# Kernel optimization log

Measured on AMD Instinct MI355X. Metric: run time of the kernel, lower is better.

The kernel has to match this reference:

```python
import jax, jax.numpy as jnp
import numpy as np

N, T, D, H, DA = 128, 256, 512, 512, 4


def setup_inputs() -> dict:
    key = jax.random.key(0)
    k1, k2, k3, k4, k5, k6 = jax.random.split(key, 6)
    x = jax.random.normal(k1, (N, T, D), dtype=jnp.float32)
    A = jax.random.normal(k2, (N, H, DA, DA), dtype=jnp.float32)
    Wx = jax.random.normal(k3, (D, 4 * H), dtype=jnp.float32) / np.sqrt(D).astype(np.float32)
    Wh = jax.random.normal(k4, (H, 4 * H), dtype=jnp.float32) / np.sqrt(H).astype(np.float32)
    Wattn = jax.random.normal(k5, (H, 4 * H), dtype=jnp.float32) / np.sqrt(H).astype(np.float32)
    b = jnp.zeros((4 * H,), dtype=jnp.float32)
    return {"x": x, "A": A, "Wx": Wx, "Wh": Wh, "Wattn": Wattn, "b": b}


def _attn(prev_h, A_flat, scale):
    # prev_h: (N,H), A_flat: (N,H,P) with P = DA*DA
    scores = jnp.einsum('nh,nhp->np', prev_h, A_flat) * scale      # (N,P)
    w = jax.nn.softmax(scores, axis=-1)                             # (N,P)
    attn = jnp.einsum('nhp,np->nh', A_flat, w)                      # (N,H)
    return attn


def reference(x, A, Wx, Wh, Wattn, b):
    n, t, d = x.shape
    h_dim = A.shape[1]
    scale = 1.0 / jnp.sqrt(jnp.asarray(h_dim, dtype=x.dtype))
    A_flat = A.reshape(n, h_dim, -1)
    h0 = jnp.mean(A, axis=(2, 3))  # (N,H)
    c0 = h0
    xs = jnp.moveaxis(x, 1, 0)     # (T,N,D)

    def step(carry, x_t):
        prev_h, prev_c = carry
        attn = _attn(prev_h, A_flat, scale)
        a = x_t @ Wx + prev_h @ Wh + attn @ Wattn + b  # (N,4H)
        i, f, o, g = jnp.split(a, 4, axis=-1)
        next_c = jax.nn.sigmoid(f) * prev_c + jax.nn.sigmoid(i) * jnp.tanh(g)
        next_h = jax.nn.sigmoid(o) * jnp.tanh(next_c)
        return (next_h, next_c), next_h

    _, hs = jax.lax.scan(step, (h0, c0), xs)  # hs: (T,N,H)
    return jnp.moveaxis(hs, 0, 1)             # (N,T,H)
```

## Files before the change

### kernel.cpp

```cpp
#include <hip/hip_runtime.h>
#include <hip/hip_bf16.h>

typedef __bf16 bf16_t;
typedef __bf16 bf16x8 __attribute__((ext_vector_type(8)));
typedef float  f32x4  __attribute__((ext_vector_type(4)));

#define N_    128
#define T_    256
#define D_    512
#define H_    512
#define G4    2048
#define ZB_ELEMS 131072
#define XF_PER_T 65536
#define WB_PER_CB 32768

__device__ __forceinline__ int zidx(int k, int n) {
  return ((((k >> 5) * 8 + (n >> 4)) * 64) + ((k >> 3) & 3) * 16 + (n & 15)) * 8 + (k & 7);
}

__device__ __forceinline__ float sigf(float x) { return 1.f / (1.f + __expf(-x)); }
__device__ __forceinline__ float tanhfast(float x) {
  float e = __expf(2.f * x);
  return 1.f - 2.f / (e + 1.f);
}

__device__ __forceinline__ bf16x8 ld_frag_llc(const bf16_t* p) {
  unsigned long long lo = __hip_atomic_load((const unsigned long long*)p,
      __ATOMIC_RELAXED, __HIP_MEMORY_SCOPE_AGENT);
  unsigned long long hi = __hip_atomic_load(((const unsigned long long*)p) + 1,
      __ATOMIC_RELAXED, __HIP_MEMORY_SCOPE_AGENT);
  union { unsigned long long q[2]; bf16x8 v; } u; u.q[0] = lo; u.q[1] = hi; return u.v;
}
__device__ __forceinline__ float ld_f32_llc(const float* p) {
  return __hip_atomic_load(p, __ATOMIC_RELAXED, __HIP_MEMORY_SCOPE_AGENT);
}
__device__ __forceinline__ void st_u32_llc(unsigned int* p, unsigned int v) {
  __hip_atomic_store(p, v, __ATOMIC_RELAXED, __HIP_MEMORY_SCOPE_AGENT);
}
__device__ __forceinline__ int ld_i32_llc(const int* p) {
  return __hip_atomic_load(p, __ATOMIC_RELAXED, __HIP_MEMORY_SCOPE_AGENT);
}
__device__ __forceinline__ unsigned int pack2bf(float lo, float hi) {
  union { bf16_t h[2]; unsigned int u; } q;
  q.h[0] = (bf16_t)lo; q.h[1] = (bf16_t)hi; return q.u;
}

__global__ void prepW_kernel(const float* __restrict__ Wh, const float* __restrict__ Wx,
                             bf16_t* __restrict__ Wb) {
  int cb = blockIdx.x >> 1, kq = blockIdx.x & 1;
  int tt = threadIdx.x;
  int hl = tt & 7, gate = (tt >> 3) & 3, ko = tt >> 5;
  int oc = gate * H_ + cb * 8 + hl;
  int jpl = hl * 4 + gate;
  int wcl = jpl >> 4, c = jpl & 15;
  for (int kb = kq * 64; kb < kq * 64 + 64; kb++) {
    int k = kb * 8 + ko;
    float v = (k < 512) ? Wh[(size_t)k * G4 + oc] : Wx[(size_t)(k - 512) * G4 + oc];
    int kk = k >> 5, ch = (k >> 3) & 3, e = k & 7;
    Wb[(size_t)cb * WB_PER_CB + (((kk * 2 + wcl) * 64) + ch * 16 + c) * 8 + e] = (bf16_t)v;
  }
}

__global__ void prepX_kernel(const float* __restrict__ x, bf16_t* __restrict__ Xf) {
  int gid = blockIdx.x * 256 + threadIdx.x;
  int e8 = gid & 63;
  int n  = (gid >> 6) & 127;
  int t  = gid >> 13;
  int k  = e8 * 8;
  const float* xp = x + ((size_t)n * T_ + t) * D_ + k;
  union { bf16_t b[8]; bf16x8 v; } u;
#pragma unroll
  for (int e = 0; e < 8; e++) u.b[e] = (bf16_t)xp[e];
  int idx = ((k >> 5) * 8 + (n >> 4)) * 64 + ((k >> 3) & 3) * 16 + (n & 15);
  ((bf16x8*)(Xf + (size_t)t * XF_PER_T))[idx] = u.v;
}

__global__ void prepA_kernel(const float* __restrict__ A, const float* __restrict__ x,
                             bf16_t* __restrict__ A_sc, float* __restrict__ cbuf,
                             bf16_t* __restrict__ Zb, float* __restrict__ S,
                             int* __restrict__ bar) {
  __shared__ float a_ld[8192];
  __shared__ float h0s[512];
  __shared__ float redb[256 * 16];
  int n = blockIdx.x, tid = threadIdx.x;
  if (n == 0 && tid < 144) bar[tid * 32] = 0;
  if (tid < 16) S[2048 + n * 16 + tid] = 0.f;
  for (int i = tid; i < 8192; i += 256) a_ld[i] = A[(size_t)n * 8192 + i];
  __syncthreads();
  for (int h = tid; h < H_; h += 256) {
    float s = 0.f;
#pragma unroll
    for (int p = 0; p < 16; p++) s += a_ld[h * 16 + p];
    s *= (1.f / 16.f);
    h0s[h] = s;
    cbuf[n * H_ + h] = s;
    Zb[zidx(h, n)] = (bf16_t)s;
  }
  for (int d = tid; d < D_; d += 256)
    Zb[zidx(512 + d, n)] = (bf16_t)x[(size_t)n * T_ * D_ + d];
  for (int idx = tid; idx < 8192; idx += 256) {
    int k = idx >> 4, p = idx & 15;
    A_sc[(size_t)n * 8192 + ((k >> 3) * 16 + p) * 8 + (k & 7)] = (bf16_t)a_ld[idx];
  }
  __syncthreads();
  float part[16];
#pragma unroll
  for (int p = 0; p < 16; p++) part[p] = 0.f;
  for (int h = tid; h < H_; h += 256) {
    float hv = h0s[h];
#pragma unroll
    for (int p = 0; p < 16; p++) part[p] += hv * a_ld[h * 16 + p];
  }
#pragma unroll
  for (int p = 0; p < 16; p++) redb[tid * 16 + p] = part[p];
  __syncthreads();
  if (tid < 16) {
    float s = 0.f;
    for (int i = 0; i < 256; i++) s += redb[i * 16 + tid];
    S[n * 16 + tid] = s;
  }
}

__global__ void __launch_bounds__(256) prepB_kernel(const float* __restrict__ Wattn,
                             const bf16_t* __restrict__ A_sc, bf16_t* __restrict__ Bg) {
  __shared__ bf16_t Al[8192];
  int n = blockIdx.x >> 2, jpQ = blockIdx.x & 3;
  int tid = threadIdx.x, p = tid & 15, jg = tid >> 4;
  for (int i = tid; i < 1024; i += 256)
    ((bf16x8*)Al)[i] = ((const bf16x8*)(A_sc + (size_t)n * 8192))[i];
  __syncthreads();
  int cbb = jpQ * 16 + jg;
  float acc[32];
#pragma unroll
  for (int j = 0; j < 32; j++) acc[j] = 0.f;
  for (int k = 0; k < 512; k++) {
    float a = (float)Al[((k >> 3) * 16 + p) * 8 + (k & 7)];
    const float* wr = Wattn + (size_t)k * G4 + cbb * 8;
#pragma unroll
    for (int gate = 0; gate < 4; gate++) {
      const float4* w4 = (const float4*)(wr + gate * H_);
      float4 wa = w4[0], wb = w4[1];
      acc[0 * 4 + gate] += a * wa.x; acc[1 * 4 + gate] += a * wa.y;
      acc[2 * 4 + gate] += a * wa.z; acc[3 * 4 + gate] += a * wa.w;
      acc[4 * 4 + gate] += a * wb.x; acc[5 * 4 + gate] += a * wb.y;
      acc[6 * 4 + gate] += a * wb.z; acc[7 * 4 + gate] += a * wb.w;
    }
  }
  bf16_t* dst = Bg + (((size_t)n * 64 + cbb) * 32) * 16 + p;
#pragma unroll
  for (int jj = 0; jj < 32; jj++) dst[jj * 16] = (bf16_t)acc[jj];
}

__device__ __forceinline__ void gridbar(int* gbase, int leaf, int g0l) {
  __syncthreads();
  if (threadIdx.x == 0) {
    int my = __hip_atomic_fetch_add(gbase + leaf * 32, 1, __ATOMIC_RELAXED, __HIP_MEMORY_SCOPE_AGENT);
    bool rootwin = false;
    if ((my & 7) == 7) {
      int r = __hip_atomic_fetch_add(gbase + 8 * 32, 1, __ATOMIC_RELAXED, __HIP_MEMORY_SCOPE_AGENT);
      if ((r & 7) == 7) {
        rootwin = true;
#pragma unroll
        for (int l = 0; l < 8; l++)
          st_u32_llc((unsigned int*)(gbase + (9 + l) * 32), (unsigned int)(g0l + 1));
      }
    }
    if (!rootwin) {
      while (ld_i32_llc(gbase + (9 + leaf) * 32) == g0l) __builtin_amdgcn_s_sleep(1);
    }
  }
  __syncthreads();
}

template<int USE_XF>
__global__ void __launch_bounds__(256, 2)
lstm_kernel(const bf16_t* __restrict__ Xf, const bf16_t* __restrict__ A_sc,
            const bf16_t* __restrict__ Wb, const bf16_t* __restrict__ Bg,
            const float* __restrict__ bvec, const float* __restrict__ cbuf,
            bf16_t* __restrict__ Zb, float* __restrict__ S,
            float* __restrict__ out, int* __restrict__ bar,
            const float* __restrict__ x) {
  __shared__ bf16_t Wl[32768];
  __shared__ f32x4 red[4][2][64];
  __shared__ float hsh[16 * 9];
  __shared__ float wls[16 * 17];

  const int wg = blockIdx.x, tid = threadIdx.x;
  const int cb = wg >> 3;
  const int grp = (wg & 7) ^ ((wg >> 3) & 7) ^ ((wg >> 6) & 7);
  const int wave = tid >> 6, lane = tid & 63;
  const int s  = grp * 16 + (lane & 15);
  const int hcE = cb * 8 + wave * 4 + (lane >> 4);
  const int jpE = cb * 32 + wave * 16 + (lane & 15);
  const float bias_l = (wave < 2) ? bvec[(jpE & 3) * H_ + (jpE >> 2)] : 0.f;
  const int jl = wave * 16 + (lane & 15);
  const int leaf = cb >> 3;
  int* gbase = bar + grp * 18 * 32;
  const int kkb = wave * 8;

  {
    const bf16x8* src = (const bf16x8*)(Wb + (size_t)cb * WB_PER_CB);
    bf16x8* dst = (bf16x8*)Wl;
    for (int i = tid; i < 4096; i += 256) dst[i] = src[i];
  }
  float creg = (wave < 2) ? cbuf[s * H_ + hcE] : 0.f;
  __syncthreads();

  int cur = 0;
  for (int t = 0; t < T_; t++) {
    const bf16_t* Zc = Zb + cur * ZB_ELEMS;
    bf16_t* Zn = Zb + (cur ^ 1) * ZB_ELEMS;
    const int cur3 = t % 3, nxt3 = (t + 1) % 3, z3 = (t + 2) % 3;

    int g0l = 0;
    if (tid == 0) g0l = ld_i32_llc(gbase + (9 + leaf) * 32);
    asm volatile("" ::: "memory");

    if (tid < 4) st_u32_llc((unsigned int*)(S + z3 * 2048 + grp * 256 + cb * 4 + tid), 0u);

    if (!USE_XF && t + 1 < T_ && tid < 64) {
      int nl = tid >> 2, e2 = (tid & 3) * 2;
      int n = grp * 16 + nl;
      const float* xp = x + ((size_t)n * T_ + (t + 1)) * D_ + cb * 8 + e2;
      st_u32_llc((unsigned int*)(Zn + zidx(512 + cb * 8 + e2, n)), pack2bf(xp[0], xp[1]));
    }

    bf16x8 afrag[8];
    if (USE_XF && wave >= 2) {
      const bf16x8* xf = (const bf16x8*)(Xf + (size_t)t * XF_PER_T);
#pragma unroll
      for (int i = 0; i < 8; i++)
        afrag[i] = xf[((kkb - 16 + i) * 8 + grp) * 64 + lane];
    } else {
#pragma unroll
      for (int i = 0; i < 8; i++)
        afrag[i] = ld_frag_llc(Zc + ((size_t)((kkb + i) * 8 + grp) * 64 + lane) * 8);
    }

    if ((tid & 63) < 4) {
      int nl = wave * 4 + (tid & 63);
      int ng = grp * 16 + nl;
      float r[16];
#pragma unroll
      for (int p = 0; p < 16; p++)
        r[p] = ld_f32_llc(S + cur3 * 2048 + ng * 16 + p) * 0.044194173824159216f;
      float m = r[0];
#pragma unroll
      for (int p = 1; p < 16; p++) m = fmaxf(m, r[p]);
      float ssum = 0.f;
#pragma unroll
      for (int p = 0; p < 16; p++) { r[p] = __expf(r[p] - m); ssum += r[p]; }
      float inv = 1.f / ssum;
#pragma unroll
      for (int p = 0; p < 16; p++) wls[nl * 17 + p] = r[p] * inv;
    }

    f32x4 acc0 = {0.f, 0.f, 0.f, 0.f}, acc1 = {0.f, 0.f, 0.f, 0.f};
    {
      const bf16x8* Wf = (const bf16x8*)Wl;
#pragma unroll
      for (int i = 0; i < 8; i++) {
        int kk = kkb + i;
        acc0 = __builtin_amdgcn_mfma_f32_16x16x32_bf16(afrag[i], Wf[(kk * 2 + 0) * 64 + lane], acc0, 0, 0, 0);
        acc1 = __builtin_amdgcn_mfma_f32_16x16x32_bf16(afrag[i], Wf[(kk * 2 + 1) * 64 + lane], acc1, 0, 0, 0);
      }
    }
    red[wave][0][lane] = acc0;
    red[wave][1][lane] = acc1;
    __syncthreads();

    if (wave < 2) {
      f32x4 fa = red[0][wave][lane];
#pragma unroll
      for (int w = 1; w < 4; w++) {
        f32x4 o = red[w][wave][lane];
        fa[0] += o[0]; fa[1] += o[1]; fa[2] += o[2]; fa[3] += o[3];
      }
      const int nl0 = (lane >> 4) << 2;
#pragma unroll
      for (int rp = 0; rp < 4; rp++) {
        int nl = nl0 + rp;
        const bf16x8* bl = (const bf16x8*)(Bg +
            (((size_t)(grp * 16 + nl) * 64 + cb) * 32 + jl) * 16);
        bf16x8 b0 = bl[0], b1 = bl[1];
        const float* wn = wls + nl * 17;
        float add = 0.f;
#pragma unroll
        for (int p = 0; p < 8; p++) add += wn[p] * (float)b0[p];
#pragma unroll
        for (int p = 0; p < 8; p++) add += wn[8 + p] * (float)b1[p];
        fa[rp] += add + bias_l;
      }

      float gv[4] = {0.f, 0.f, 0.f, 0.f};
      const int srcbase = ((lane >> 2) & 3) * 16 + (lane >> 4) * 4;
#pragma unroll
      for (int rp = 0; rp < 4; rp++) {
        float v = fa[rp];
#pragma unroll
        for (int g = 0; g < 4; g++) {
          float sv = __shfl(v, srcbase + g, 64);
          if ((lane & 3) == rp) gv[g] = sv;
        }
      }

      float si = sigf(gv[0]), sf = sigf(gv[1]), so = sigf(gv[2]);
      float cn = sf * creg + si * tanhfast(gv[3]);
      float hn = so * tanhfast(cn);
      creg = cn;
      __builtin_nontemporal_store(hn, out + ((size_t)s * T_ + t) * H_ + hcE);

      union { bf16_t h; unsigned short u; } cvt; cvt.h = (bf16_t)hn;
      unsigned int hbits = cvt.u;
      unsigned int other = __shfl(hbits, (lane + 16) & 63, 64);
      if (((lane >> 4) & 1) == 0)
        st_u32_llc((unsigned int*)(Zn + zidx(hcE, s)), hbits | (other << 16));
      hsh[(s & 15) * 9 + (hcE & 7)] = hn;
    }
    __syncthreads();

    if (t + 1 < T_) {
      int nl = tid >> 4, p = tid & 15;
      int ng = grp * 16 + nl;
      const bf16x8 av = *(const bf16x8*)(A_sc + ((size_t)ng * 64 + cb) * 128 + p * 8);
      float part = 0.f;
#pragma unroll
      for (int c = 0; c < 8; c++) part += hsh[nl * 9 + c] * (float)av[c];
      atomicAdd(S + nxt3 * 2048 + ng * 16 + p, part);
    }

    gridbar(gbase, leaf, g0l);
    cur ^= 1;
  }
}

extern "C" void kernel_launch(void* const* d_in, const int* in_sizes, int n_in,
                              void* d_out, int out_size, void* d_ws, size_t ws_size,
                              hipStream_t stream) {
  const float* x     = (const float*)d_in[0];
  const float* A     = (const float*)d_in[1];
  const float* Wx    = (const float*)d_in[2];
  const float* Wh    = (const float*)d_in[3];
  const float* Wattn = (const float*)d_in[4];
  const float* bv    = (const float*)d_in[5];
  float* out = (float*)d_out;

  char* ws = (char*)d_ws;
  const size_t BAR_OFF = 0;
  const size_t S_OFF   = 32768;
  const size_t CB_OFF  = 57344;
  const size_t ZB_OFF  = 319488;
  const size_t ASC_OFF = 843776;
  const size_t WB_OFF  = 2940928;
  const size_t BG_OFF  = 7135232;
  const size_t XF_OFF  = 15523840;
  const size_t WS_BASE = 15523840;
  const size_t WS_XF   = 49078272;
  if (ws_size < WS_BASE) return;
  const bool use_xf = (ws_size >= WS_XF);

  int*    bar  = (int*)(ws + BAR_OFF);
  float*  S    = (float*)(ws + S_OFF);
  float*  cbuf = (float*)(ws + CB_OFF);
  bf16_t* Zb   = (bf16_t*)(ws + ZB_OFF);
  bf16_t* A_sc = (bf16_t*)(ws + ASC_OFF);
  bf16_t* Wb   = (bf16_t*)(ws + WB_OFF);
  bf16_t* Bg   = (bf16_t*)(ws + BG_OFF);
  bf16_t* Xf   = (bf16_t*)(ws + XF_OFF);

  prepW_kernel<<<dim3(128), dim3(256), 0, stream>>>(Wh, Wx, Wb);
  prepA_kernel<<<dim3(128), dim3(256), 0, stream>>>(A, x, A_sc, cbuf, Zb, S, bar);
  prepB_kernel<<<dim3(512), dim3(256), 0, stream>>>(Wattn, A_sc, Bg);
  if (use_xf) {
    prepX_kernel<<<dim3(8192), dim3(256), 0, stream>>>(x, Xf);
    lstm_kernel<1><<<dim3(512), dim3(256), 0, stream>>>(Xf, A_sc, Wb, Bg, bv, cbuf, Zb, S, out, bar, x);
  } else {
    lstm_kernel<0><<<dim3(512), dim3(256), 0, stream>>>(Xf, A_sc, Wb, Bg, bv, cbuf, Zb, S, out, bar, x);
  }
}
```

Measured before the change: 1.902 ms.

## Use two-wave workgroups with full-K MFMA per wave and split score accumulators

Each workgroup drops from four waves splitting K with a shared-memory reduction to two waves that each own one 16-column output tile and run all 32 K-steps. This removes the LDS reduction of partial accumulators, and every wave now does gate math instead of only half of them. The attention score buffer is split into 8 partitions indexed by cb&7, which spreads atomicAdd contention; readers then sum the 8 partials before the softmax. In exchange, each wave carries a longer serial MFMA chain and more fragment registers, occupancy drops, and score reads grow eightfold, which could lengthen the per-step critical path.

```diff
diff --git a/kernel.cpp b/kernel.cpp
--- a/kernel.cpp
+++ b/kernel.cpp
@@ -13,6 +13,7 @@
 #define ZB_ELEMS 131072
 #define XF_PER_T 65536
 #define WB_PER_CB 32768
+#define SPH 16384
 
 __device__ __forceinline__ int zidx(int k, int n) {
   return ((((k >> 5) * 8 + (n >> 4)) * 64) + ((k >> 3) & 3) * 16 + (n & 15)) * 8 + (k & 7);
@@ -84,7 +85,11 @@
   __shared__ float redb[256 * 16];
   int n = blockIdx.x, tid = threadIdx.x;
   if (n == 0 && tid < 144) bar[tid * 32] = 0;
-  if (tid < 16) S[2048 + n * 16 + tid] = 0.f;
+  if (tid < 128) S[SPH + (tid >> 4) * 2048 + n * 16 + (tid & 15)] = 0.f;
+  if (tid >= 128 && tid < 240) {
+    int q = 1 + ((tid - 128) >> 4);
+    S[q * 2048 + n * 16 + (tid & 15)] = 0.f;
+  }
   for (int i = tid; i < 8192; i += 256) a_ld[i] = A[(size_t)n * 8192 + i];
   __syncthreads();
   for (int h = tid; h < H_; h += 256) {
@@ -173,7 +178,7 @@
 }
 
 template<int USE_XF>
-__global__ void __launch_bounds__(256, 2)
+__global__ void __launch_bounds__(128, 1)
 lstm_kernel(const bf16_t* __restrict__ Xf, const bf16_t* __restrict__ A_sc,
             const bf16_t* __restrict__ Wb, const bf16_t* __restrict__ Bg,
             const float* __restrict__ bvec, const float* __restrict__ cbuf,
@@ -181,7 +186,7 @@
             float* __restrict__ out, int* __restrict__ bar,
             const float* __restrict__ x) {
   __shared__ bf16_t Wl[32768];
-  __shared__ f32x4 red[4][2][64];
+  __shared__ float sraw[16 * 17];
   __shared__ float hsh[16 * 9];
   __shared__ float wls[16 * 17];
 
@@ -192,18 +197,17 @@
   const int s  = grp * 16 + (lane & 15);
   const int hcE = cb * 8 + wave * 4 + (lane >> 4);
   const int jpE = cb * 32 + wave * 16 + (lane & 15);
-  const float bias_l = (wave < 2) ? bvec[(jpE & 3) * H_ + (jpE >> 2)] : 0.f;
+  const float bias_l = bvec[(jpE & 3) * H_ + (jpE >> 2)];
   const int jl = wave * 16 + (lane & 15);
   const int leaf = cb >> 3;
   int* gbase = bar + grp * 18 * 32;
-  const int kkb = wave * 8;
 
   {
     const bf16x8* src = (const bf16x8*)(Wb + (size_t)cb * WB_PER_CB);
     bf16x8* dst = (bf16x8*)Wl;
-    for (int i = tid; i < 4096; i += 256) dst[i] = src[i];
-  }
-  float creg = (wave < 2) ? cbuf[s * H_ + hcE] : 0.f;
+    for (int i = tid; i < 4096; i += 128) dst[i] = src[i];
+  }
+  float creg = cbuf[s * H_ + hcE];
   __syncthreads();
 
   int cur = 0;
@@ -216,7 +220,8 @@
     if (tid == 0) g0l = ld_i32_llc(gbase + (9 + leaf) * 32);
     asm volatile("" ::: "memory");
 
-    if (tid < 4) st_u32_llc((unsigned int*)(S + z3 * 2048 + grp * 256 + cb * 4 + tid), 0u);
+    if (tid < 32)
+      st_u32_llc((unsigned int*)(S + (size_t)z3 * SPH + (cb >> 3) * 2048 + grp * 256 + (cb & 7) * 32 + tid), 0u);
 
     if (!USE_XF && t + 1 < T_ && tid < 64) {
       int nl = tid >> 2, e2 = (tid & 3) * 2;
@@ -225,25 +230,38 @@
       st_u32_llc((unsigned int*)(Zn + zidx(512 + cb * 8 + e2, n)), pack2bf(xp[0], xp[1]));
     }
 
-    bf16x8 afrag[8];
-    if (USE_XF && wave >= 2) {
+    bf16x8 af[16], ax[16];
+#pragma unroll
+    for (int i = 0; i < 16; i++)
+      af[i] = ld_frag_llc(Zc + ((size_t)(i * 8 + grp) * 64 + lane) * 8);
+    if (USE_XF) {
       const bf16x8* xf = (const bf16x8*)(Xf + (size_t)t * XF_PER_T);
 #pragma unroll
-      for (int i = 0; i < 8; i++)
-        afrag[i] = xf[((kkb - 16 + i) * 8 + grp) * 64 + lane];
+      for (int i = 0; i < 16; i++)
+        ax[i] = xf[(i * 8 + grp) * 64 + lane];
     } else {
 #pragma unroll
-      for (int i = 0; i < 8; i++)
-        afrag[i] = ld_frag_llc(Zc + ((size_t)((kkb + i) * 8 + grp) * 64 + lane) * 8);
-    }
-
-    if ((tid & 63) < 4) {
-      int nl = wave * 4 + (tid & 63);
-      int ng = grp * 16 + nl;
+      for (int i = 0; i < 16; i++)
+        ax[i] = ld_frag_llc(Zc + ((size_t)((16 + i) * 8 + grp) * 64 + lane) * 8);
+    }
+
+#pragma unroll
+    for (int u = 0; u < 2; u++) {
+      int idx = tid + u * 128;
+      int nl = idx >> 4, p = idx & 15;
+      const float* sp = S + (size_t)cur3 * SPH + (grp * 16 + nl) * 16 + p;
+      float sum = 0.f;
+#pragma unroll
+      for (int q = 0; q < 8; q++) sum += ld_f32_llc(sp + q * 2048);
+      sraw[nl * 17 + p] = sum;
+    }
+    __syncthreads();
+
+    if (lane < 8) {
+      int nl = wave * 8 + lane;
       float r[16];
 #pragma unroll
-      for (int p = 0; p < 16; p++)
-        r[p] = ld_f32_llc(S + cur3 * 2048 + ng * 16 + p) * 0.044194173824159216f;
+      for (int p = 0; p < 16; p++) r[p] = sraw[nl * 17 + p] * 0.044194173824159216f;
       float m = r[0];
 #pragma unroll
       for (int p = 1; p < 16; p++) m = fmaxf(m, r[p]);
@@ -255,27 +273,19 @@
       for (int p = 0; p < 16; p++) wls[nl * 17 + p] = r[p] * inv;
     }
 
-    f32x4 acc0 = {0.f, 0.f, 0.f, 0.f}, acc1 = {0.f, 0.f, 0.f, 0.f};
+    f32x4 acc = {0.f, 0.f, 0.f, 0.f};
     {
       const bf16x8* Wf = (const bf16x8*)Wl;
 #pragma unroll
-      for (int i = 0; i < 8; i++) {
-        int kk = kkb + i;
-        acc0 = __builtin_amdgcn_mfma_f32_16x16x32_bf16(afrag[i], Wf[(kk * 2 + 0) * 64 + lane], acc0, 0, 0, 0);
-        acc1 = __builtin_amdgcn_mfma_f32_16x16x32_bf16(afrag[i], Wf[(kk * 2 + 1) * 64 + lane], acc1, 0, 0, 0);
-      }
-    }
-    red[wave][0][lane] = acc0;
-    red[wave][1][lane] = acc1;
+      for (int i = 0; i < 16; i++)
+        acc = __builtin_amdgcn_mfma_f32_16x16x32_bf16(af[i], Wf[(i * 2 + wave) * 64 + lane], acc, 0, 0, 0);
+#pragma unroll
+      for (int i = 0; i < 16; i++)
+        acc = __builtin_amdgcn_mfma_f32_16x16x32_bf16(ax[i], Wf[((16 + i) * 2 + wave) * 64 + lane], acc, 0, 0, 0);
+    }
     __syncthreads();
 
-    if (wave < 2) {
-      f32x4 fa = red[0][wave][lane];
-#pragma unroll
-      for (int w = 1; w < 4; w++) {
-        f32x4 o = red[w][wave][lane];
-        fa[0] += o[0]; fa[1] += o[1]; fa[2] += o[2]; fa[3] += o[3];
-      }
+    {
       const int nl0 = (lane >> 4) << 2;
 #pragma unroll
       for (int rp = 0; rp < 4; rp++) {
@@ -289,14 +299,14 @@
         for (int p = 0; p < 8; p++) add += wn[p] * (float)b0[p];
 #pragma unroll
         for (int p = 0; p < 8; p++) add += wn[8 + p] * (float)b1[p];
-        fa[rp] += add + bias_l;
+        acc[rp] += add + bias_l;
       }
 
       float gv[4] = {0.f, 0.f, 0.f, 0.f};
       const int srcbase = ((lane >> 2) & 3) * 16 + (lane >> 4) * 4;
 #pragma unroll
       for (int rp = 0; rp < 4; rp++) {
-        float v = fa[rp];
+        float v = acc[rp];
 #pragma unroll
         for (int g = 0; g < 4; g++) {
           float sv = __shfl(v, srcbase + g, 64);
@@ -320,13 +330,18 @@
     __syncthreads();
 
     if (t + 1 < T_) {
-      int nl = tid >> 4, p = tid & 15;
-      int ng = grp * 16 + nl;
-      const bf16x8 av = *(const bf16x8*)(A_sc + ((size_t)ng * 64 + cb) * 128 + p * 8);
-      float part = 0.f;
-#pragma unroll
-      for (int c = 0; c < 8; c++) part += hsh[nl * 9 + c] * (float)av[c];
-      atomicAdd(S + nxt3 * 2048 + ng * 16 + p, part);
+      float* Sn = S + (size_t)nxt3 * SPH + (cb & 7) * 2048;
+#pragma unroll
+      for (int u = 0; u < 2; u++) {
+        int idx = tid + u * 128;
+        int nl = idx >> 4, p = idx & 15;
+        int ng = grp * 16 + nl;
+        const bf16x8 av = *(const bf16x8*)(A_sc + ((size_t)ng * 64 + cb) * 128 + p * 8);
+        float part = 0.f;
+#pragma unroll
+        for (int c = 0; c < 8; c++) part += hsh[nl * 9 + c] * (float)av[c];
+        atomicAdd(Sn + ng * 16 + p, part);
+      }
     }
 
     gridbar(gbase, leaf, g0l);
@@ -348,14 +363,14 @@
   char* ws = (char*)d_ws;
   const size_t BAR_OFF = 0;
   const size_t S_OFF   = 32768;
-  const size_t CB_OFF  = 57344;
-  const size_t ZB_OFF  = 319488;
-  const size_t ASC_OFF = 843776;
-  const size_t WB_OFF  = 2940928;
-  const size_t BG_OFF  = 7135232;
-  const size_t XF_OFF  = 15523840;
-  const size_t WS_BASE = 15523840;
-  const size_t WS_XF   = 49078272;
+  const size_t CB_OFF  = 229376;
+  const size_t ZB_OFF  = 491520;
+  const size_t ASC_OFF = 1015808;
+  const size_t WB_OFF  = 3112960;
+  const size_t BG_OFF  = 7307264;
+  const size_t XF_OFF  = 15695872;
+  const size_t WS_BASE = 15695872;
+  const size_t WS_XF   = 49250304;
   if (ws_size < WS_BASE) return;
   const bool use_xf = (ws_size >= WS_XF);
 
@@ -373,8 +388,8 @@
   prepB_kernel<<<dim3(512), dim3(256), 0, stream>>>(Wattn, A_sc, Bg);
   if (use_xf) {
     prepX_kernel<<<dim3(8192), dim3(256), 0, stream>>>(x, Xf);
-    lstm_kernel<1><<<dim3(512), dim3(256), 0, stream>>>(Xf, A_sc, Wb, Bg, bv, cbuf, Zb, S, out, bar, x);
+    lstm_kernel<1><<<dim3(512), dim3(128), 0, stream>>>(Xf, A_sc, Wb, Bg, bv, cbuf, Zb, S, out, bar, x);
   } else {
-    lstm_kernel<0><<<dim3(512), dim3(256), 0, stream>>>(Xf, A_sc, Wb, Bg, bv, cbuf, Zb, S, out, bar, x);
-  }
-}
+    lstm_kernel<0><<<dim3(512), dim3(128), 0, stream>>>(Xf, A_sc, Wb, Bg, bv, cbuf, Zb, S, out, bar, x);
+  }
+}
```

Measured after the change: 2.636 ms. 38.6% more time.
